# Kernel optimization log

Measured on AMD Instinct MI355X. Metric: run time of the kernel, lower is better.

## Reference

```python
import jax, jax.numpy as jnp
import numpy as np

B, T, D, P, C = 65536, 3, 512, 32, 10  # batch, views, x_dim, p_dim, num_classes

def setup_inputs() -> dict:
    key = jax.random.key(0)
    ks = jax.random.split(key, 6)
    return {
        "x": jax.random.normal(ks[0], (B, T, D), dtype=jnp.float32),
        "Wk": jax.random.normal(ks[1], (P, D), dtype=jnp.float32) * (1.0 / np.sqrt(D)),
        "Wv": jax.random.normal(ks[2], (P, D), dtype=jnp.float32) * (1.0 / np.sqrt(D)),
        "Wq": jax.random.normal(ks[3], (P, T * D), dtype=jnp.float32) * (1.0 / np.sqrt(T * D)),
        "Wfc": jax.random.normal(ks[4], (C, P), dtype=jnp.float32) * (1.0 / np.sqrt(P)),
        "bfc": jax.random.normal(ks[5], (C,), dtype=jnp.float32) * 0.01,
    }

def reference(x, Wk, Wv, Wq, Wfc, bfc):
    # x: [B, 3, D]. Per-sample: k_i = Wk x_i, v_i = Wv x_i, q = Wq concat(x1,x2,x3)
    k = jnp.einsum('btd,pd->btp', x, Wk)                 # [B,3,P]
    v = jnp.einsum('btd,pd->btp', x, Wv)                 # [B,3,P]
    q = jnp.einsum('bf,pf->bp', x.reshape(x.shape[0], -1), Wq)  # [B,P]
    a = jax.nn.softmax(jnp.einsum('bp,btp->bt', q, k), axis=-1)  # 3-way softmax [B,3]
    c = jnp.einsum('bt,btp->bp', a, v)                   # weighted sum [B,P]
    return c @ Wfc.T + bfc                               # [B,C]
```

## Files before the change

kernel.cpp:

```cpp
#include <hip/hip_runtime.h>


typedef __attribute__((ext_vector_type(4))) float  f32x4;
typedef __attribute__((ext_vector_type(8))) _Float16 h16x8;

#define T_VIEWS 3
#define D_DIM   512
#define P_DIM   32
#define C_DIM   10
#define NROWS   80
#define M_WAVE  16
#define WAVES_PER_BLOCK 4

__global__ void build_weights(const float* __restrict__ Wk,
                              const float* __restrict__ Wv,
                              const float* __restrict__ Wq,
                              const float* __restrict__ Wfc,
                              _Float16* __restrict__ Wc) {
    const int row = blockIdx.x;
    const int t   = row / NROWS;
    const int j   = row % NROWS;
    const int d   = threadIdx.x;
    float val;
    if (j < 32) {
        val = Wk[j * D_DIM + d];
    } else if (j < 64) {
        const int p = j - 32;
        val = Wq[p * (T_VIEWS * D_DIM) + t * D_DIM + d];
    } else if (j < 64 + C_DIM) {
        const int i = j - 64;
        float s = 0.f;
        #pragma unroll
        for (int p = 0; p < P_DIM; ++p)
            s += Wfc[i * P_DIM + p] * Wv[p * D_DIM + d];
        val = s;
    } else {
        val = 0.f;
    }
    Wc[(size_t)row * D_DIM + d] = (_Float16)val;
}

__global__ __launch_bounds__(256) void attn_fused(
        const float* __restrict__ x,
        const _Float16* __restrict__ Wc,
        const float* __restrict__ bfc,
        float* __restrict__ out) {
    const int lane = threadIdx.x & 63;
    const int wave = threadIdx.x >> 6;
    const int col  = lane & 15;
    const int quad = lane >> 4;
    const int row_base = blockIdx.x * (M_WAVE * WAVES_PER_BLOCK) + wave * M_WAVE;

    f32x4 acc[3][5];
    #pragma unroll
    for (int t = 0; t < 3; ++t)
        #pragma unroll
        for (int n = 0; n < 5; ++n)
            acc[t][n] = (f32x4)0.f;

    const float* xrow = x + (size_t)(row_base + col) * (T_VIEWS * D_DIM) + quad * 8;

    #pragma unroll
    for (int t = 0; t < 3; ++t) {
        const float* xt = xrow + t * D_DIM;
        const _Float16* wt = Wc + ((size_t)t * NROWS + col) * D_DIM + quad * 8;
        #pragma unroll 4
        for (int kc = 0; kc < 16; ++kc) {
            const f32x4 x0 = *(const f32x4*)(xt + kc * 32);
            const f32x4 x1 = *(const f32x4*)(xt + kc * 32 + 4);
            h16x8 a;
            #pragma unroll
            for (int i = 0; i < 4; ++i) {
                a[i]     = (_Float16)x0[i];
                a[i + 4] = (_Float16)x1[i];
            }
            #pragma unroll
            for (int n = 0; n < 5; ++n) {
                const h16x8 b = *(const h16x8*)(wt + kc * 32 + (size_t)n * 16 * D_DIM);
                acc[t][n] = __builtin_amdgcn_mfma_f32_16x16x32_f16(a, b, acc[t][n], 0, 0, 0);
            }
        }
    }

    const float bias = (col < C_DIM) ? bfc[col] : 0.f;

    float outv[4];
    #pragma unroll
    for (int r = 0; r < 4; ++r) {
        const float qa = acc[0][2][r] + acc[1][2][r] + acc[2][2][r];
        const float qb = acc[0][3][r] + acc[1][3][r] + acc[2][3][r];
        float s0 = qa * acc[0][0][r] + qb * acc[0][1][r];
        float s1 = qa * acc[1][0][r] + qb * acc[1][1][r];
        float s2 = qa * acc[2][0][r] + qb * acc[2][1][r];
        #pragma unroll
        for (int m = 1; m <= 8; m <<= 1) {
            s0 += __shfl_xor(s0, m, 64);
            s1 += __shfl_xor(s1, m, 64);
            s2 += __shfl_xor(s2, m, 64);
        }
        const float mx = fmaxf(s0, fmaxf(s1, s2));
        const float e0 = __expf(s0 - mx);
        const float e1 = __expf(s1 - mx);
        const float e2 = __expf(s2 - mx);
        const float inv = 1.f / (e0 + e1 + e2);
        outv[r] = (e0 * acc[0][4][r] + e1 * acc[1][4][r] + e2 * acc[2][4][r]) * inv + bias;
    }

    if (col < C_DIM) {
        const int b0 = row_base + quad * 4;
        #pragma unroll
        for (int r = 0; r < 4; ++r)
            out[(size_t)(b0 + r) * C_DIM + col] = outv[r];
    }
}

extern "C" void kernel_launch(void* const* d_in, const int* in_sizes, int n_in,
                              void* d_out, int out_size, void* d_ws, size_t ws_size,
                              hipStream_t stream) {
    const float* x   = (const float*)d_in[0];
    const float* Wk  = (const float*)d_in[1];
    const float* Wv  = (const float*)d_in[2];
    const float* Wq  = (const float*)d_in[3];
    const float* Wfc = (const float*)d_in[4];
    const float* bfc = (const float*)d_in[5];
    _Float16* Wc = (_Float16*)d_ws;

    hipLaunchKernelGGL(build_weights, dim3(T_VIEWS * NROWS), dim3(D_DIM), 0, stream,
                       Wk, Wv, Wq, Wfc, Wc);

    const int B_TOTAL = in_sizes[0] / (T_VIEWS * D_DIM);
    const int blocks = B_TOTAL / (M_WAVE * WAVES_PER_BLOCK);
    hipLaunchKernelGGL(attn_fused, dim3(blocks), dim3(256), 0, stream,
                       x, Wc, bfc, (float*)d_out);
}
```

Before: 587.5 us.

## Pre-swizzle weights into MFMA fragment layout and process two M-tiles per wave

The weight build kernel now writes the fp16 combined weights in the exact per-lane MFMA B-fragment order, so each lane loads its B operand with one contiguous 16-byte access. The main kernel handles two 16-sample tiles per wave and reuses each loaded B fragment across both, halving weight load traffic per sample. The x activations are read with nontemporal loads to avoid polluting cache. The cost is doubled accumulator register use (30 f32x4) and half as many blocks, which may reduce occupancy and latency hiding on this memory-bound kernel.

```diff
diff --git a/kernel.cpp b/kernel.cpp
--- a/kernel.cpp
+++ b/kernel.cpp
@@ -9,14 +9,18 @@
 #define P_DIM   32
 #define C_DIM   10
 #define NROWS   80
-#define M_WAVE  16
+#define NT      5
+#define KC      16
+#define M_TILES 2
+#define M_WAVE  (M_TILES*16)
 #define WAVES_PER_BLOCK 4
+#define SAMPLES_PER_BLOCK (M_WAVE*WAVES_PER_BLOCK)
 
 __global__ void build_weights(const float* __restrict__ Wk,
                               const float* __restrict__ Wv,
                               const float* __restrict__ Wq,
                               const float* __restrict__ Wfc,
-                              _Float16* __restrict__ Wc) {
+                              _Float16* __restrict__ Wf) {
     const int row = blockIdx.x;
     const int t   = row / NROWS;
     const int j   = row % NROWS;
@@ -37,80 +41,92 @@
     } else {
         val = 0.f;
     }
-    Wc[(size_t)row * D_DIM + d] = (_Float16)val;
+    const int n = j >> 4, col = j & 15;
+    const int kc = d >> 5, r = d & 31, quad = r >> 3, jj = r & 7;
+    const size_t addr = (size_t)((((t * KC + kc) * NT + n) * 64) + quad * 16 + col) * 8 + jj;
+    Wf[addr] = (_Float16)val;
 }
 
 __global__ __launch_bounds__(256) void attn_fused(
         const float* __restrict__ x,
-        const _Float16* __restrict__ Wc,
+        const _Float16* __restrict__ Wf,
         const float* __restrict__ bfc,
         float* __restrict__ out) {
     const int lane = threadIdx.x & 63;
     const int wave = threadIdx.x >> 6;
     const int col  = lane & 15;
     const int quad = lane >> 4;
-    const int row_base = blockIdx.x * (M_WAVE * WAVES_PER_BLOCK) + wave * M_WAVE;
+    const int row_base = blockIdx.x * SAMPLES_PER_BLOCK + wave * M_WAVE;
 
-    f32x4 acc[3][5];
+    f32x4 acc[3][M_TILES][NT];
     #pragma unroll
     for (int t = 0; t < 3; ++t)
         #pragma unroll
-        for (int n = 0; n < 5; ++n)
-            acc[t][n] = (f32x4)0.f;
+        for (int m = 0; m < M_TILES; ++m)
+            #pragma unroll
+            for (int n = 0; n < NT; ++n)
+                acc[t][m][n] = (f32x4)0.f;
 
-    const float* xrow = x + (size_t)(row_base + col) * (T_VIEWS * D_DIM) + quad * 8;
+    const float* xbase = x + (size_t)(row_base + col) * (T_VIEWS * D_DIM) + quad * 8;
 
     #pragma unroll
     for (int t = 0; t < 3; ++t) {
-        const float* xt = xrow + t * D_DIM;
-        const _Float16* wt = Wc + ((size_t)t * NROWS + col) * D_DIM + quad * 8;
-        #pragma unroll 4
-        for (int kc = 0; kc < 16; ++kc) {
-            const f32x4 x0 = *(const f32x4*)(xt + kc * 32);
-            const f32x4 x1 = *(const f32x4*)(xt + kc * 32 + 4);
-            h16x8 a;
+        const _Float16* wt = Wf + (size_t)t * (KC * NT * 512) + lane * 8;
+        #pragma unroll 2
+        for (int kc = 0; kc < KC; ++kc) {
+            h16x8 b[NT];
             #pragma unroll
-            for (int i = 0; i < 4; ++i) {
-                a[i]     = (_Float16)x0[i];
-                a[i + 4] = (_Float16)x1[i];
-            }
+            for (int n = 0; n < NT; ++n)
+                b[n] = *(const h16x8*)(wt + (kc * NT + n) * 512);
             #pragma unroll
-            for (int n = 0; n < 5; ++n) {
-                const h16x8 b = *(const h16x8*)(wt + kc * 32 + (size_t)n * 16 * D_DIM);
-                acc[t][n] = __builtin_amdgcn_mfma_f32_16x16x32_f16(a, b, acc[t][n], 0, 0, 0);
+            for (int m = 0; m < M_TILES; ++m) {
+                const float* xp = xbase + t * D_DIM + (size_t)m * 16 * (T_VIEWS * D_DIM) + kc * 32;
+                const f32x4 x0 = __builtin_nontemporal_load((const f32x4*)xp);
+                const f32x4 x1 = __builtin_nontemporal_load((const f32x4*)(xp + 4));
+                h16x8 a;
+                #pragma unroll
+                for (int i = 0; i < 4; ++i) {
+                    a[i]     = (_Float16)x0[i];
+                    a[i + 4] = (_Float16)x1[i];
+                }
+                #pragma unroll
+                for (int n = 0; n < NT; ++n)
+                    acc[t][m][n] = __builtin_amdgcn_mfma_f32_16x16x32_f16(a, b[n], acc[t][m][n], 0, 0, 0);
             }
         }
     }
 
     const float bias = (col < C_DIM) ? bfc[col] : 0.f;
 
-    float outv[4];
     #pragma unroll
-    for (int r = 0; r < 4; ++r) {
-        const float qa = acc[0][2][r] + acc[1][2][r] + acc[2][2][r];
-        const float qb = acc[0][3][r] + acc[1][3][r] + acc[2][3][r];
-        float s0 = qa * acc[0][0][r] + qb * acc[0][1][r];
-        float s1 = qa * acc[1][0][r] + qb * acc[1][1][r];
-        float s2 = qa * acc[2][0][r] + qb * acc[2][1][r];
+    for (int m = 0; m < M_TILES; ++m) {
+        float outv[4];
         #pragma unroll
-        for (int m = 1; m <= 8; m <<= 1) {
-            s0 += __shfl_xor(s0, m, 64);
-            s1 += __shfl_xor(s1, m, 64);
-            s2 += __shfl_xor(s2, m, 64);
+        for (int r = 0; r < 4; ++r) {
+            const float qa = acc[0][m][2][r] + acc[1][m][2][r] + acc[2][m][2][r];
+            const float qb = acc[0][m][3][r] + acc[1][m][3][r] + acc[2][m][3][r];
+            float s0 = qa * acc[0][m][0][r] + qb * acc[0][m][1][r];
+            float s1 = qa * acc[1][m][0][r] + qb * acc[1][m][1][r];
+            float s2 = qa * acc[2][m][0][r] + qb * acc[2][m][1][r];
+            #pragma unroll
+            for (int msk = 1; msk <= 8; msk <<= 1) {
+                s0 += __shfl_xor(s0, msk, 64);
+                s1 += __shfl_xor(s1, msk, 64);
+                s2 += __shfl_xor(s2, msk, 64);
+            }
+            const float mx = fmaxf(s0, fmaxf(s1, s2));
+            const float e0 = __expf(s0 - mx);
+            const float e1 = __expf(s1 - mx);
+            const float e2 = __expf(s2 - mx);
+            const float inv = 1.f / (e0 + e1 + e2);
+            outv[r] = (e0 * acc[0][m][4][r] + e1 * acc[1][m][4][r] + e2 * acc[2][m][4][r]) * inv + bias;
         }
-        const float mx = fmaxf(s0, fmaxf(s1, s2));
-        const float e0 = __expf(s0 - mx);
-        const float e1 = __expf(s1 - mx);
-        const float e2 = __expf(s2 - mx);
-        const float inv = 1.f / (e0 + e1 + e2);
-        outv[r] = (e0 * acc[0][4][r] + e1 * acc[1][4][r] + e2 * acc[2][4][r]) * inv + bias;
-    }
-
-    if (col < C_DIM) {
-        const int b0 = row_base + quad * 4;
-        #pragma unroll
-        for (int r = 0; r < 4; ++r)
-            out[(size_t)(b0 + r) * C_DIM + col] = outv[r];
+        if (col < C_DIM) {
+            const int b0 = row_base + m * 16 + quad * 4;
+            #pragma unroll
+            for (int r = 0; r < 4; ++r)
+                out[(size_t)(b0 + r) * C_DIM + col] = outv[r];
+        }
     }
 }
 
@@ -123,13 +139,13 @@
     const float* Wq  = (const float*)d_in[3];
     const float* Wfc = (const float*)d_in[4];
     const float* bfc = (const float*)d_in[5];
-    _Float16* Wc = (_Float16*)d_ws;
+    _Float16* Wf = (_Float16*)d_ws;
 
     hipLaunchKernelGGL(build_weights, dim3(T_VIEWS * NROWS), dim3(D_DIM), 0, stream,
-                       Wk, Wv, Wq, Wfc, Wc);
+                       Wk, Wv, Wq, Wfc, Wf);
 
     const int B_TOTAL = in_sizes[0] / (T_VIEWS * D_DIM);
-    const int blocks = B_TOTAL / (M_WAVE * WAVES_PER_BLOCK);
+    const int blocks = B_TOTAL / SAMPLES_PER_BLOCK;
     hipLaunchKernelGGL(attn_fused, dim3(blocks), dim3(256), 0, stream,
-                       x, Wc, bfc, (float*)d_out);
+                       x, Wf, bfc, (float*)d_out);
 }
```

After: 536.7 us. 8.6% less time.
